# Kernel tuning notes

Measured on AMD Instinct MI355X. Metric: run time of the kernel, lower is better.

## Reference

```python
import jax, jax.numpy as jnp
import numpy as np

N_NODES = 50000
N_EDGES = 800000
VOCAB = 1001  # input_dim + 1
HID = 128
OUT = 40
N_LAYERS = 3


def setup_inputs() -> dict:
    key = jax.random.key(0)
    ks = jax.random.split(key, 10)
    feats = jax.random.randint(ks[0], (N_NODES, 2), 0, VOCAB, dtype=jnp.int32)
    src = jax.random.randint(ks[1], (N_EDGES,), 0, N_NODES, dtype=jnp.int32)
    dst = jax.random.randint(ks[2], (N_EDGES,), 0, N_NODES, dtype=jnp.int32)
    s = 1.0 / np.sqrt(HID)
    key_emb = jax.random.normal(ks[3], (VOCAB, HID), jnp.float32)
    val_emb = jax.random.normal(ks[4], (VOCAB, HID), jnp.float32)
    W1 = jax.random.uniform(ks[5], (N_LAYERS, HID, HID), jnp.float32, -s, s)
    b1 = jnp.zeros((N_LAYERS, HID), jnp.float32)
    W2 = jax.random.uniform(ks[6], (N_LAYERS, HID, HID), jnp.float32, -s, s)
    b2 = jnp.zeros((N_LAYERS, HID), jnp.float32)
    Wc = jax.random.uniform(ks[7], (OUT, HID), jnp.float32, -s, s)
    return {"feats": feats, "src": src, "dst": dst, "key_emb": key_emb,
            "val_emb": val_emb, "W1": W1, "b1": b1, "W2": W2, "b2": b2, "Wc": Wc}


def reference(feats, src, dst, key_emb, val_emb, W1, b1, W2, b2, Wc):
    # embedding sum + ReLU: [N, HID]
    h = jax.nn.relu(key_emb[feats[:, 0]] + val_emb[feats[:, 1]])
    for i in range(N_LAYERS):
        # GIN sum aggregation: scatter-add src features to dst; eps = 0
        agg = jax.ops.segment_sum(h[src], dst, num_segments=N_NODES)
        z = h + agg
        # 2-layer MLP (norm='none'): Linear -> ReLU -> Linear
        z = jax.nn.relu(z @ W1[i].T + b1[i])
        h = z @ W2[i].T + b2[i]
        # dropout p=0 -> identity
    return h @ Wc.T
```

## Files before the change

### kernel.cpp

```cpp
#include <hip/hip_runtime.h>

#define N_NODES 50000
#define N_PAD 50048
#define N_EDGES 800000
#define HID 128
#define NBUCK 782
#define BUCK_CAP 2048
#define ESC_CHUNK 2048
#define ESC_NCHUNK ((N_EDGES + ESC_CHUNK - 1) / ESC_CHUNK)

typedef unsigned int uint;
typedef __attribute__((ext_vector_type(8))) short short8;
typedef __attribute__((ext_vector_type(4))) float f32x4;

__device__ inline uint f2bf_pair(float x, float y) {
    uint ux = __float_as_uint(x);
    uint uy = __float_as_uint(y);
    ux = (ux + 0x7FFFu + ((ux >> 16) & 1u)) >> 16;
    uy = (uy + 0x7FFFu + ((uy >> 16) & 1u)) >> 16;
    return ux | (uy << 16);
}
__device__ inline float bf_lo(uint v) { return __uint_as_float(v << 16); }
__device__ inline float bf_hi(uint v) { return __uint_as_float(v & 0xFFFF0000u); }

__global__ __launch_bounds__(256) void edge_scatter_kernel(const int* __restrict__ src,
                                                           const int* __restrict__ dst,
                                                           int* __restrict__ cursor16,
                                                           uint* __restrict__ col_tmp) {
    int cls = blockIdx.x & 7;
    int base = (blockIdx.x >> 3) * ESC_CHUNK;
#pragma unroll
    for (int i = 0; i < ESC_CHUNK / 256; ++i) {
        int e = base + i * 256 + threadIdx.x;
        if (e < N_EDGES) {
            int d = dst[e];
            int s = src[e];
            int b = d >> 6;
            uint val = (uint)s | ((uint)(d & 63) << 16);
            if ((b & 7) == cls) {
                int p = atomicAdd(&cursor16[b * 16], 1);
                if (p < BUCK_CAP)
                    col_tmp[(size_t)b * BUCK_CAP + p] = val;
            }
        }
    }
}

__global__ __launch_bounds__(256) void bucket_build_kernel(const int* __restrict__ cursor16,
                                                           uint* __restrict__ col_tmp,
                                                           int* __restrict__ row_start,
                                                           int* __restrict__ counts) {
    __shared__ uint edges[BUCK_CAP];
    __shared__ int cnt64[64], pre64[64], cur64[64];
    int b = blockIdx.x, t = threadIdx.x;
    int cnt = cursor16[b * 16];
    if (cnt > BUCK_CAP) cnt = BUCK_CAP;
    uint* region = col_tmp + (size_t)b * BUCK_CAP;
    for (int i = t; i < cnt; i += 256) edges[i] = region[i];
    if (t < 64) { cnt64[t] = 0; cur64[t] = 0; }
    __syncthreads();
    for (int i = t; i < cnt; i += 256) atomicAdd(&cnt64[edges[i] >> 16], 1);
    __syncthreads();
    if (t == 0) {
        int s = 0;
        for (int j = 0; j < 64; ++j) { pre64[j] = s; s += cnt64[j]; }
    }
    __syncthreads();
    for (int i = t; i < cnt; i += 256) {
        uint e = edges[i];
        int dl = e >> 16;
        int p = atomicAdd(&cur64[dl], 1);
        region[pre64[dl] + p] = e & 0xFFFFu;
    }
    if (t < 64) {
        int node = b * 64 + t;
        row_start[node] = b * BUCK_CAP + pre64[t];
        counts[node] = cnt64[t];
    }
}

__global__ void wconv_kernel(const float* __restrict__ W1, const float* __restrict__ W2,
                             const float* __restrict__ Wc,
                             uint* __restrict__ w1b, uint* __restrict__ w2b,
                             uint* __restrict__ wcb) {
    int i = blockIdx.x * 256 + threadIdx.x;
    if (i < 3 * 128 * 64) {
        w1b[i] = f2bf_pair(W1[2 * i], W1[2 * i + 1]);
        w2b[i] = f2bf_pair(W2[2 * i], W2[2 * i + 1]);
    }
    if (i < 48 * 64) {
        int r = i >> 6, q = i & 63;
        wcb[i] = (r < 40) ? f2bf_pair(Wc[r * 128 + 2 * q], Wc[r * 128 + 2 * q + 1]) : 0u;
    }
}

__global__ void embed_kernel(const int* __restrict__ feats, const float* __restrict__ key_emb,
                             const float* __restrict__ val_emb, uint* __restrict__ h) {
    int idx = blockIdx.x * 256 + threadIdx.x;
    if (idx >= N_NODES * 32) return;
    int n = idx >> 5, q = idx & 31;
    int f0 = feats[2 * n], f1 = feats[2 * n + 1];
    float4 a = ((const float4*)key_emb)[f0 * 32 + q];
    float4 b = ((const float4*)val_emb)[f1 * 32 + q];
    float r0 = fmaxf(a.x + b.x, 0.f), r1 = fmaxf(a.y + b.y, 0.f);
    float r2 = fmaxf(a.z + b.z, 0.f), r3 = fmaxf(a.w + b.w, 0.f);
    uint2 o;
    o.x = f2bf_pair(r0, r1);
    o.y = f2bf_pair(r2, r3);
    *(uint2*)&h[(size_t)n * 64 + q * 2] = o;
}

__global__ __launch_bounds__(256) void agg_kernel(const uint* __restrict__ hb,
                                                  uint* __restrict__ zb,
                                                  const int* __restrict__ row_start,
                                                  const int* __restrict__ counts,
                                                  const uint* __restrict__ col) {
    int node = blockIdx.x * 4 + (threadIdx.x >> 6);
    int l = threadIdx.x & 63;
    int half = l >> 5, fl = l & 31;
    const uint2* hp2 = (const uint2*)hb;
    int s = __builtin_amdgcn_readfirstlane(row_start[node]);
    int c = __builtin_amdgcn_readfirstlane(counts[node]);
    float a0 = 0.f, a1 = 0.f, a2 = 0.f, a3 = 0.f;
    int j = 0;
    for (; j + 8 <= c; j += 8) {
        int u0 = col[s + j + half];
        int u1 = col[s + j + 2 + half];
        int u2 = col[s + j + 4 + half];
        int u3 = col[s + j + 6 + half];
        uint2 v0 = hp2[(size_t)u0 * 32 + fl];
        uint2 v1 = hp2[(size_t)u1 * 32 + fl];
        uint2 v2 = hp2[(size_t)u2 * 32 + fl];
        uint2 v3 = hp2[(size_t)u3 * 32 + fl];
        a0 += (bf_lo(v0.x) + bf_lo(v1.x)) + (bf_lo(v2.x) + bf_lo(v3.x));
        a1 += (bf_hi(v0.x) + bf_hi(v1.x)) + (bf_hi(v2.x) + bf_hi(v3.x));
        a2 += (bf_lo(v0.y) + bf_lo(v1.y)) + (bf_lo(v2.y) + bf_lo(v3.y));
        a3 += (bf_hi(v0.y) + bf_hi(v1.y)) + (bf_hi(v2.y) + bf_hi(v3.y));
    }
    for (; j + 2 <= c; j += 2) {
        int u = col[s + j + half];
        uint2 v = hp2[(size_t)u * 32 + fl];
        a0 += bf_lo(v.x); a1 += bf_hi(v.x); a2 += bf_lo(v.y); a3 += bf_hi(v.y);
    }
    if (j < c && half == 0) {
        int u = col[s + j];
        uint2 v = hp2[(size_t)u * 32 + fl];
        a0 += bf_lo(v.x); a1 += bf_hi(v.x); a2 += bf_lo(v.y); a3 += bf_hi(v.y);
    }
    a0 += __shfl_xor(a0, 32);
    a1 += __shfl_xor(a1, 32);
    a2 += __shfl_xor(a2, 32);
    a3 += __shfl_xor(a3, 32);
    if (half == 0) {
        uint2 hv = hp2[(size_t)node * 32 + fl];
        a0 += bf_lo(hv.x); a1 += bf_hi(hv.x); a2 += bf_lo(hv.y); a3 += bf_hi(hv.y);
        uint2 o;
        o.x = f2bf_pair(a0, a1);
        o.y = f2bf_pair(a2, a3);
        ((uint2*)zb)[(size_t)node * 32 + fl] = o;
    }
}

template <bool LAST>
__global__ __launch_bounds__(256) void mlp_kernel(
    const uint* __restrict__ zb, uint* __restrict__ hout,
    const uint* __restrict__ w1b, const float* __restrict__ b1,
    const uint* __restrict__ w2b, const float* __restrict__ b2,
    const uint* __restrict__ wcb, float* __restrict__ out) {
    __shared__ float z1[64][132];
    int t = threadIdx.x;
    int w = t >> 6, l = t & 63;
    int lm = l & 15, lk = l >> 4;
    int row0 = blockIdx.x * 64;

    f32x4 acc[8];
#pragma unroll
    for (int n = 0; n < 8; ++n) {
        float bv = b1[n * 16 + lm];
        acc[n] = (f32x4){bv, bv, bv, bv};
    }
#pragma unroll
    for (int ks = 0; ks < 4; ++ks) {
        uint4 av = *(const uint4*)(zb + (size_t)(row0 + w * 16 + lm) * 64 + ks * 16 + lk * 4);
        short8 a = *(short8*)&av;
#pragma unroll
        for (int n = 0; n < 8; ++n) {
            uint4 bv4 = *(const uint4*)(w1b + (size_t)(n * 16 + lm) * 64 + ks * 16 + lk * 4);
            short8 b = *(short8*)&bv4;
            acc[n] = __builtin_amdgcn_mfma_f32_16x16x32_bf16(a, b, acc[n], 0, 0, 0);
        }
    }
#pragma unroll
    for (int n = 0; n < 8; ++n)
#pragma unroll
        for (int q = 0; q < 4; ++q)
            z1[w * 16 + lk * 4 + q][n * 16 + lm] = fmaxf(acc[n][q], 0.f);

#pragma unroll
    for (int n = 0; n < 8; ++n) {
        float bv = b2[n * 16 + lm];
        acc[n] = (f32x4){bv, bv, bv, bv};
    }
#pragma unroll
    for (int ks = 0; ks < 4; ++ks) {
        float4 f0 = *(const float4*)&z1[w * 16 + lm][ks * 32 + lk * 8];
        float4 f1 = *(const float4*)&z1[w * 16 + lm][ks * 32 + lk * 8 + 4];
        uint4 ua;
        ua.x = f2bf_pair(f0.x, f0.y);
        ua.y = f2bf_pair(f0.z, f0.w);
        ua.z = f2bf_pair(f1.x, f1.y);
        ua.w = f2bf_pair(f1.z, f1.w);
        short8 a = *(short8*)&ua;
#pragma unroll
        for (int n = 0; n < 8; ++n) {
            uint4 bv4 = *(const uint4*)(w2b + (size_t)(n * 16 + lm) * 64 + ks * 16 + lk * 4);
            short8 b = *(short8*)&bv4;
            acc[n] = __builtin_amdgcn_mfma_f32_16x16x32_bf16(a, b, acc[n], 0, 0, 0);
        }
    }
#pragma unroll
    for (int n = 0; n < 8; ++n)
#pragma unroll
        for (int q = 0; q < 4; ++q)
            z1[w * 16 + lk * 4 + q][n * 16 + lm] = acc[n][q];

    if constexpr (!LAST) {
        __syncthreads();
        for (int i = t; i < 2048; i += 256) {
            int row = i >> 5, j = i & 31;
            float4 v = *(const float4*)&z1[row][j * 4];
            uint2 o;
            o.x = f2bf_pair(v.x, v.y);
            o.y = f2bf_pair(v.z, v.w);
            *(uint2*)&hout[(size_t)(row0 + row) * 64 + j * 2] = o;
        }
    } else {
        f32x4 acc3[3];
#pragma unroll
        for (int n = 0; n < 3; ++n) acc3[n] = (f32x4){0.f, 0.f, 0.f, 0.f};
#pragma unroll
        for (int ks = 0; ks < 4; ++ks) {
            float4 f0 = *(const float4*)&z1[w * 16 + lm][ks * 32 + lk * 8];
            float4 f1 = *(const float4*)&z1[w * 16 + lm][ks * 32 + lk * 8 + 4];
            uint4 ua;
            ua.x = f2bf_pair(f0.x, f0.y);
            ua.y = f2bf_pair(f0.z, f0.w);
            ua.z = f2bf_pair(f1.x, f1.y);
            ua.w = f2bf_pair(f1.z, f1.w);
            short8 a = *(short8*)&ua;
#pragma unroll
            for (int n = 0; n < 3; ++n) {
                uint4 bv4 = *(const uint4*)(wcb + (size_t)(n * 16 + lm) * 64 + ks * 16 + lk * 4);
                short8 b = *(short8*)&bv4;
                acc3[n] = __builtin_amdgcn_mfma_f32_16x16x32_bf16(a, b, acc3[n], 0, 0, 0);
            }
        }
#pragma unroll
        for (int n = 0; n < 3; ++n) {
            int cc = n * 16 + lm;
            if (cc < 40) {
#pragma unroll
                for (int q = 0; q < 4; ++q) {
                    int node = row0 + w * 16 + lk * 4 + q;
                    if (node < N_NODES) out[(size_t)node * 40 + cc] = acc3[n][q];
                }
            }
        }
    }
}

extern "C" void kernel_launch(void* const* d_in, const int* in_sizes, int n_in,
                              void* d_out, int out_size, void* d_ws, size_t ws_size,
                              hipStream_t stream) {
    const int* feats = (const int*)d_in[0];
    const int* src = (const int*)d_in[1];
    const int* dst = (const int*)d_in[2];
    const float* key_emb = (const float*)d_in[3];
    const float* val_emb = (const float*)d_in[4];
    const float* W1 = (const float*)d_in[5];
    const float* b1 = (const float*)d_in[6];
    const float* W2 = (const float*)d_in[7];
    const float* b2 = (const float*)d_in[8];
    const float* Wc = (const float*)d_in[9];
    float* out = (float*)d_out;

    char* ws = (char*)d_ws;
    auto carve = [&](size_t bytes) {
        char* p = ws;
        ws += (bytes + 255) & ~(size_t)255;
        return p;
    };
    uint* h0 = (uint*)carve((size_t)N_PAD * 64 * 4);
    uint* h1 = (uint*)carve((size_t)N_PAD * 64 * 4);
    uint* zb = (uint*)carve((size_t)N_PAD * 64 * 4);
    uint* w1b = (uint*)carve((size_t)3 * 128 * 64 * 4);
    uint* w2b = (uint*)carve((size_t)3 * 128 * 64 * 4);
    uint* wcb = (uint*)carve((size_t)48 * 64 * 4);
    int* row_start = (int*)carve((size_t)N_PAD * 4);
    int* counts = (int*)carve((size_t)N_PAD * 4);
    int* cursor16 = (int*)carve((size_t)NBUCK * 16 * 4);
    uint* col_tmp = (uint*)carve((size_t)NBUCK * BUCK_CAP * 4);

    hipMemsetAsync(cursor16, 0, (size_t)NBUCK * 16 * 4, stream);

    edge_scatter_kernel<<<ESC_NCHUNK * 8, 256, 0, stream>>>(src, dst, cursor16, col_tmp);
    bucket_build_kernel<<<NBUCK, 256, 0, stream>>>(cursor16, col_tmp, row_start, counts);

    wconv_kernel<<<(3 * 128 * 64 + 255) / 256, 256, 0, stream>>>(W1, W2, Wc, w1b, w2b, wcb);
    embed_kernel<<<(N_NODES * 32 + 255) / 256, 256, 0, stream>>>(feats, key_emb, val_emb, h0);

    const int NBLK_MLP = (N_PAD + 63) / 64;
    const int NBLK_AGG = (N_NODES + 3) / 4;

    agg_kernel<<<NBLK_AGG, 256, 0, stream>>>(h0, zb, row_start, counts, col_tmp);
    mlp_kernel<false><<<NBLK_MLP, 256, 0, stream>>>(zb, h1, w1b, b1, w2b, b2, nullptr, nullptr);
    agg_kernel<<<NBLK_AGG, 256, 0, stream>>>(h1, zb, row_start, counts, col_tmp);
    mlp_kernel<false><<<NBLK_MLP, 256, 0, stream>>>(zb, h0, w1b + 128 * 64, b1 + HID,
                                                    w2b + 128 * 64, b2 + HID, nullptr, nullptr);
    agg_kernel<<<NBLK_AGG, 256, 0, stream>>>(h0, zb, row_start, counts, col_tmp);
    mlp_kernel<true><<<NBLK_MLP, 256, 0, stream>>>(zb, nullptr, w1b + 2 * 128 * 64, b1 + 2 * HID,
                                                   w2b + 2 * 128 * 64, b2 + 2 * HID, wcb, out);
}
```

Baseline: 341.5 us.

## Use block-local shared-memory binning with coarser buckets for CSR build

Replaces the 8-way class-filtered edge scatter, which made every edge-chunk read eight times and did one global atomic per edge, with a single pass per chunk. Each block bins edges into shared-memory bins for 98 coarse buckets of 512 nodes and reserves global space with one atomic per bucket per block, so global atomics and redundant dst/src reads drop. The bucket build now uses 512 threads and a parallel scan over 512 local nodes. Risks: per-bucket capacity of 8704 may overflow for skewed graphs (edges silently dropped), and the 98 build blocks give less parallelism.

```diff
diff --git a/kernel.cpp b/kernel.cpp
--- a/kernel.cpp
+++ b/kernel.cpp
@@ -4,8 +4,9 @@
 #define N_PAD 50048
 #define N_EDGES 800000
 #define HID 128
-#define NBUCK 782
-#define BUCK_CAP 2048
+#define NBUCK 98
+#define BUCK_CAP 8704
+#define LBIN_CAP 48
 #define ESC_CHUNK 2048
 #define ESC_NCHUNK ((N_EDGES + ESC_CHUNK - 1) / ESC_CHUNK)
 
@@ -23,59 +24,87 @@
 __device__ inline float bf_lo(uint v) { return __uint_as_float(v << 16); }
 __device__ inline float bf_hi(uint v) { return __uint_as_float(v & 0xFFFF0000u); }
 
-__global__ __launch_bounds__(256) void edge_scatter_kernel(const int* __restrict__ src,
-                                                           const int* __restrict__ dst,
-                                                           int* __restrict__ cursor16,
-                                                           uint* __restrict__ col_tmp) {
-    int cls = blockIdx.x & 7;
-    int base = (blockIdx.x >> 3) * ESC_CHUNK;
+__global__ __launch_bounds__(256) void bin_scatter_kernel(const int* __restrict__ src,
+                                                          const int* __restrict__ dst,
+                                                          int* __restrict__ gcursor,
+                                                          uint* __restrict__ col_tmp) {
+    __shared__ uint lbin[NBUCK][LBIN_CAP];
+    __shared__ int lcnt[NBUCK], gbase[NBUCK];
+    int t = threadIdx.x;
+    int base = blockIdx.x * ESC_CHUNK;
+    if (t < NBUCK) lcnt[t] = 0;
+    __syncthreads();
 #pragma unroll
     for (int i = 0; i < ESC_CHUNK / 256; ++i) {
-        int e = base + i * 256 + threadIdx.x;
+        int e = base + i * 256 + t;
         if (e < N_EDGES) {
             int d = dst[e];
-            int s = src[e];
-            int b = d >> 6;
-            uint val = (uint)s | ((uint)(d & 63) << 16);
-            if ((b & 7) == cls) {
-                int p = atomicAdd(&cursor16[b * 16], 1);
-                if (p < BUCK_CAP)
-                    col_tmp[(size_t)b * BUCK_CAP + p] = val;
+            int b = d >> 9;
+            uint val = (uint)src[e] | ((uint)(d & 511) << 16);
+            int p = atomicAdd(&lcnt[b], 1);
+            if (p < LBIN_CAP) {
+                lbin[b][p] = val;
+            } else {
+                int gp = atomicAdd(&gcursor[b], 1);
+                if (gp < BUCK_CAP) col_tmp[(size_t)b * BUCK_CAP + gp] = val;
             }
         }
     }
-}
-
-__global__ __launch_bounds__(256) void bucket_build_kernel(const int* __restrict__ cursor16,
+    __syncthreads();
+    if (t < NBUCK) {
+        int c = lcnt[t];
+        if (c > LBIN_CAP) c = LBIN_CAP;
+        gbase[t] = atomicAdd(&gcursor[t], c);
+    }
+    __syncthreads();
+    for (int i = t; i < NBUCK * LBIN_CAP; i += 256) {
+        int b = i / LBIN_CAP, slot = i % LBIN_CAP;
+        int c = lcnt[b];
+        if (c > LBIN_CAP) c = LBIN_CAP;
+        if (slot < c) {
+            int gp = gbase[b] + slot;
+            if (gp < BUCK_CAP) col_tmp[(size_t)b * BUCK_CAP + gp] = lbin[b][slot];
+        }
+    }
+}
+
+__global__ __launch_bounds__(512) void bucket_build_kernel(const int* __restrict__ gcursor,
                                                            uint* __restrict__ col_tmp,
                                                            int* __restrict__ row_start,
                                                            int* __restrict__ counts) {
     __shared__ uint edges[BUCK_CAP];
-    __shared__ int cnt64[64], pre64[64], cur64[64];
+    __shared__ int cnt[512], pre[512], cur[512], s[512];
     int b = blockIdx.x, t = threadIdx.x;
-    int cnt = cursor16[b * 16];
-    if (cnt > BUCK_CAP) cnt = BUCK_CAP;
+    int cntE = gcursor[b];
+    if (cntE > BUCK_CAP) cntE = BUCK_CAP;
     uint* region = col_tmp + (size_t)b * BUCK_CAP;
-    for (int i = t; i < cnt; i += 256) edges[i] = region[i];
-    if (t < 64) { cnt64[t] = 0; cur64[t] = 0; }
-    __syncthreads();
-    for (int i = t; i < cnt; i += 256) atomicAdd(&cnt64[edges[i] >> 16], 1);
-    __syncthreads();
-    if (t == 0) {
-        int s = 0;
-        for (int j = 0; j < 64; ++j) { pre64[j] = s; s += cnt64[j]; }
-    }
-    __syncthreads();
-    for (int i = t; i < cnt; i += 256) {
+    for (int i = t; i < cntE; i += 512) edges[i] = region[i];
+    cnt[t] = 0;
+    cur[t] = 0;
+    __syncthreads();
+    for (int i = t; i < cntE; i += 512) atomicAdd(&cnt[edges[i] >> 16], 1);
+    __syncthreads();
+    int v = cnt[t];
+    s[t] = v;
+    __syncthreads();
+    for (int off = 1; off < 512; off <<= 1) {
+        int add = (t >= off) ? s[t - off] : 0;
+        __syncthreads();
+        s[t] += add;
+        __syncthreads();
+    }
+    pre[t] = s[t] - v;
+    __syncthreads();
+    for (int i = t; i < cntE; i += 512) {
         uint e = edges[i];
         int dl = e >> 16;
-        int p = atomicAdd(&cur64[dl], 1);
-        region[pre64[dl] + p] = e & 0xFFFFu;
-    }
-    if (t < 64) {
-        int node = b * 64 + t;
-        row_start[node] = b * BUCK_CAP + pre64[t];
-        counts[node] = cnt64[t];
+        int p = atomicAdd(&cur[dl], 1);
+        region[pre[dl] + p] = e & 0xFFFFu;
+    }
+    int node = b * 512 + t;
+    if (node < N_PAD) {
+        row_start[node] = b * BUCK_CAP + pre[t];
+        counts[node] = cnt[t];
     }
 }
 
@@ -124,10 +153,10 @@
     float a0 = 0.f, a1 = 0.f, a2 = 0.f, a3 = 0.f;
     int j = 0;
     for (; j + 8 <= c; j += 8) {
-        int u0 = col[s + j + half];
-        int u1 = col[s + j + 2 + half];
-        int u2 = col[s + j + 4 + half];
-        int u3 = col[s + j + 6 + half];
+        int u0 = (int)col[s + j + half];
+        int u1 = (int)col[s + j + 2 + half];
+        int u2 = (int)col[s + j + 4 + half];
+        int u3 = (int)col[s + j + 6 + half];
         uint2 v0 = hp2[(size_t)u0 * 32 + fl];
         uint2 v1 = hp2[(size_t)u1 * 32 + fl];
         uint2 v2 = hp2[(size_t)u2 * 32 + fl];
@@ -138,12 +167,12 @@
         a3 += (bf_hi(v0.y) + bf_hi(v1.y)) + (bf_hi(v2.y) + bf_hi(v3.y));
     }
     for (; j + 2 <= c; j += 2) {
-        int u = col[s + j + half];
+        int u = (int)col[s + j + half];
         uint2 v = hp2[(size_t)u * 32 + fl];
         a0 += bf_lo(v.x); a1 += bf_hi(v.x); a2 += bf_lo(v.y); a3 += bf_hi(v.y);
     }
     if (j < c && half == 0) {
-        int u = col[s + j];
+        int u = (int)col[s + j];
         uint2 v = hp2[(size_t)u * 32 + fl];
         a0 += bf_lo(v.x); a1 += bf_hi(v.x); a2 += bf_lo(v.y); a3 += bf_hi(v.y);
     }
@@ -298,13 +327,13 @@
     uint* wcb = (uint*)carve((size_t)48 * 64 * 4);
     int* row_start = (int*)carve((size_t)N_PAD * 4);
     int* counts = (int*)carve((size_t)N_PAD * 4);
-    int* cursor16 = (int*)carve((size_t)NBUCK * 16 * 4);
+    int* gcursor = (int*)carve(512);
     uint* col_tmp = (uint*)carve((size_t)NBUCK * BUCK_CAP * 4);
 
-    hipMemsetAsync(cursor16, 0, (size_t)NBUCK * 16 * 4, stream);
-
-    edge_scatter_kernel<<<ESC_NCHUNK * 8, 256, 0, stream>>>(src, dst, cursor16, col_tmp);
-    bucket_build_kernel<<<NBUCK, 256, 0, stream>>>(cursor16, col_tmp, row_start, counts);
+    hipMemsetAsync(gcursor, 0, 512, stream);
+
+    bin_scatter_kernel<<<ESC_NCHUNK, 256, 0, stream>>>(src, dst, gcursor, col_tmp);
+    bucket_build_kernel<<<NBUCK, 512, 0, stream>>>(gcursor, col_tmp, row_start, counts);
 
     wconv_kernel<<<(3 * 128 * 64 + 255) / 256, 256, 0, stream>>>(W1, W2, Wc, w1b, w2b, wcb);
     embed_kernel<<<(N_NODES * 32 + 255) / 256, 256, 0, stream>>>(feats, key_emb, val_emb, h0);
```

New measurement: 317.8 us. -6.9%, faster.
